# Kernel optimization log

Measured on AMD Instinct MI355X. Metric: run time of the kernel, lower is better.

The kernel has to match this reference:

```python
import jax, jax.numpy as jnp
import numpy as np

DIM, INNER, HEADS = 512, 64, 8

def setup_inputs() -> dict:
    key = jax.random.key(0)
    ks = jax.random.split(key, 9)
    s = lambda fan_in: 1.0 / np.sqrt(fan_in)
    x  = jax.random.normal(ks[0], (2, 4096, DIM), dtype=jnp.float32)
    # per-head Q/K/V projection weights (naive per-head linears in the source)
    Wq = jax.random.uniform(ks[1], (HEADS, DIM, INNER), minval=-s(DIM), maxval=s(DIM))
    Wk = jax.random.uniform(ks[2], (HEADS, DIM, INNER), minval=-s(DIM), maxval=s(DIM))
    Wv = jax.random.uniform(ks[3], (HEADS, DIM, INNER), minval=-s(DIM), maxval=s(DIM))
    bq = jax.random.uniform(ks[4], (HEADS, INNER), minval=-s(DIM), maxval=s(DIM))
    bk = jax.random.uniform(ks[5], (HEADS, INNER), minval=-s(DIM), maxval=s(DIM))
    bv = jax.random.uniform(ks[6], (HEADS, INNER), minval=-s(DIM), maxval=s(DIM))
    Wo = jax.random.uniform(ks[7], (HEADS * INNER, DIM), minval=-s(HEADS*INNER), maxval=s(HEADS*INNER))
    bo = jax.random.uniform(ks[8], (DIM,), minval=-s(HEADS*INNER), maxval=s(HEADS*INNER))
    return {"x": x, "Wq": Wq, "bq": bq, "Wk": Wk, "bk": bk, "Wv": Wv, "bv": bv, "Wo": Wo, "bo": bo}

def reference(x, Wq, bq, Wk, bk, Wv, bv, Wo, bo):
    # x: [B,S,D]; per-head projections -> [B,H,S,E]
    q = jnp.einsum('bsd,hde->bhse', x, Wq) + bq[None, :, None, :]
    k = jnp.einsum('bsd,hde->bhse', x, Wk) + bk[None, :, None, :]
    v = jnp.einsum('bsd,hde->bhse', x, Wv) + bv[None, :, None, :]
    scale = 1.0 / jnp.sqrt(jnp.asarray(q.shape[-1], q.dtype))
    scores = jnp.einsum('bhse,bhte->bhst', q, k) * scale  # [B,H,S,S]
    attn = jax.nn.softmax(scores, axis=-1)
    y = jnp.einsum('bhst,bhte->bhse', attn, v)            # [B,H,S,E]
    B, H, S, E = y.shape
    cat = jnp.transpose(y, (0, 2, 1, 3)).reshape(B, S, H * E)
    return cat @ Wo + bo
```

## Files before the change

kernel.cpp:

```cpp
#include <hip/hip_runtime.h>
#include <hip/hip_bf16.h>

typedef __attribute__((ext_vector_type(8))) short bf16x8;
typedef __attribute__((ext_vector_type(4))) float f32x4;
typedef __attribute__((ext_vector_type(16))) float f32x16;
typedef __attribute__((ext_vector_type(4))) unsigned int u32x4;

#define DIM   512
#define INNER 64
#define HEADS 8
#define BATCH 2
#define SEQ   4096
#define MTOT  (BATCH*SEQ)

__device__ __forceinline__ unsigned short f2bf(float f) {
    union { float f; unsigned u; } v; v.f = f;
    unsigned u = v.u;
    unsigned r = (u + 0x7fffu + ((u >> 16) & 1u)) >> 16;
    return (unsigned short)r;
}

__device__ __forceinline__ float bf2f(unsigned short u) {
    union { unsigned u; float f; } v; v.u = ((unsigned)u) << 16;
    return v.f;
}

__device__ __forceinline__ unsigned cvt_pk_bf16(float a, float b) {
    unsigned r;
    asm("v_cvt_pk_bf16_f32 %0, %1, %2" : "=v"(r) : "v"(a), "v"(b));
    return r;
}

#define GLOAD_LDS16(gptr, lptr)                                               \
    __builtin_amdgcn_global_load_lds(                                         \
        (const __attribute__((address_space(1))) unsigned int*)(gptr),        \
        (__attribute__((address_space(3))) unsigned int*)(lptr), 16, 0, 0)

__global__ void convert_kernel(const float* __restrict__ x,
                               const float* __restrict__ Wq,
                               const float* __restrict__ Wk,
                               const float* __restrict__ Wv,
                               const float* __restrict__ Wo,
                               unsigned short* __restrict__ xb,
                               unsigned short* __restrict__ wt,
                               unsigned short* __restrict__ wot) {
    const int total_x = MTOT * DIM / 4;
    const int total_w = 1536 * 512;
    const int total_o = 512 * 512;
    const int total   = total_x + total_w + total_o;
    for (int i = blockIdx.x * blockDim.x + threadIdx.x; i < total;
         i += gridDim.x * blockDim.x) {
        if (i < total_x) {
            float4 v = ((const float4*)x)[i];
            ushort4 o4;
            o4.x = f2bf(v.x); o4.y = f2bf(v.y); o4.z = f2bf(v.z); o4.w = f2bf(v.w);
            ((ushort4*)xb)[i] = o4;
        } else if (i < total_x + total_w) {
            int j = i - total_x;
            int n = j >> 9, d = j & 511;
            int proj = n >> 9, h = (n >> 6) & 7, e = n & 63;
            const float* W = (proj == 0) ? Wq : (proj == 1) ? Wk : Wv;
            wt[j] = f2bf(W[((size_t)h * 512 + d) * 64 + e]);
        } else {
            int j = i - total_x - total_w;
            int n = j >> 9, d = j & 511;
            wot[j] = f2bf(Wo[(size_t)d * 512 + n]);
        }
    }
}

__global__ __launch_bounds__(256) void qkv_gemm(
        const unsigned short* __restrict__ xb,
        const unsigned short* __restrict__ wt,
        const float* __restrict__ bq, const float* __restrict__ bk,
        const float* __restrict__ bv,
        unsigned short* __restrict__ Q, unsigned short* __restrict__ K,
        unsigned short* __restrict__ VT) {
    __shared__ __align__(16) unsigned short As[128][64];
    __shared__ __align__(16) unsigned short Bs[128][64];
    const int m0 = blockIdx.x * 128;
    const int n0 = blockIdx.y * 128;
    const int tid = threadIdx.x;
    const int w = tid >> 6, l = tid & 63;
    const int wm = w >> 1, wn = w & 1;
    const int srow = l >> 3;
    const int cs = (l & 7) ^ srow;
    const unsigned short* aSrc = xb + (size_t)(m0 + w * 32 + srow) * 512 + cs * 8;
    const unsigned short* bSrc = wt + (size_t)(n0 + w * 32 + srow) * 512 + cs * 8;
    f32x4 acc[4][4] = {};

    for (int k0 = 0; k0 < 512; k0 += 64) {
        __syncthreads();
        #pragma unroll
        for (int g = 0; g < 4; ++g) {
            GLOAD_LDS16(aSrc + (size_t)g * 8 * 512 + k0, &As[w * 32 + g * 8][0]);
            GLOAD_LDS16(bSrc + (size_t)g * 8 * 512 + k0, &Bs[w * 32 + g * 8][0]);
        }
        __syncthreads();
        #pragma unroll
        for (int ks = 0; ks < 2; ++ks) {
            const int ccol = (((ks * 4 + (l >> 4)) ^ (l & 7))) * 8;
            bf16x8 a[4], bb[4];
            #pragma unroll
            for (int mb = 0; mb < 4; ++mb)
                a[mb] = *(const bf16x8*)(&As[wm * 64 + mb * 16 + (l & 15)][ccol]);
            #pragma unroll
            for (int nb = 0; nb < 4; ++nb)
                bb[nb] = *(const bf16x8*)(&Bs[wn * 64 + nb * 16 + (l & 15)][ccol]);
            #pragma unroll
            for (int mb = 0; mb < 4; ++mb)
                #pragma unroll
                for (int nb = 0; nb < 4; ++nb)
                    acc[mb][nb] = __builtin_amdgcn_mfma_f32_16x16x32_bf16(
                        a[mb], bb[nb], acc[mb][nb], 0, 0, 0);
        }
    }

    const float QSCALE = 0.125f * 1.4426950408889634f;
    for (int nb = 0; nb < 4; ++nb) {
        int n = n0 + wn * 64 + nb * 16 + (l & 15);
        int proj = n >> 9, h = (n >> 6) & 7, e = n & 63;
        const float* bias = (proj == 0) ? bq : (proj == 1) ? bk : bv;
        float bval = bias[h * 64 + e];
        float scl = (proj == 0) ? QSCALE : 1.0f;
        for (int mb = 0; mb < 4; ++mb) {
            for (int r = 0; r < 4; ++r) {
                int m = m0 + wm * 64 + mb * 16 + (l >> 4) * 4 + r;
                int b = m >> 12, s = m & 4095;
                unsigned short bf = f2bf((acc[mb][nb][r] + bval) * scl);
                if (proj == 0)
                    Q[((size_t)(b * 8 + h) * 4096 + s) * 64 + e] = bf;
                else if (proj == 1)
                    K[((size_t)(b * 8 + h) * 4096 + s) * 64 + e] = bf;
                else
                    VT[((size_t)(b * 8 + h) * 64 + e) * 4096 + s] = bf;
            }
        }
    }
}

template <int NSPLIT>
__global__ __launch_bounds__(256, 4) void flash_attn(
        const unsigned short* __restrict__ Q,
        const unsigned short* __restrict__ K,
        const unsigned short* __restrict__ VT,
        unsigned short* __restrict__ y,
        unsigned short* __restrict__ Opart,
        float* __restrict__ Lpart) {
    __shared__ __align__(16) unsigned short Ks[64][64];
    __shared__ __align__(16) unsigned short Vs[64][64];

    constexpr int GRP = 16 * NSPLIT;
    const int lin = blockIdx.x;
    const int g = lin & (GRP - 1);
    const int qb = lin / GRP;
    const int bh = g / NSPLIT;
    const int z = g & (NSPLIT - 1);
    const int q0 = qb * 128;
    const int TPS = 64 / NSPLIT;
    const int t0 = z * TPS;
    const int tid = threadIdx.x;
    const int w = tid >> 6, l = tid & 63;
    const int ql = l & 31, hi = l >> 5;

    const unsigned short* Qp = Q + (size_t)bh * (4096 * 64);
    const unsigned short* Kp = K + (size_t)bh * (4096 * 64);
    const unsigned short* Vp = VT + (size_t)bh * (64 * 4096);

    bf16x8 qf[4];
    const int qrow = q0 + w * 32 + ql;
    #pragma unroll
    for (int i = 0; i < 4; ++i)
        qf[i] = *(const bf16x8*)(Qp + (size_t)qrow * 64 + i * 16 + hi * 8);

    bf16x8 ones;
    #pragma unroll
    for (int i = 0; i < 8; ++i) ones[i] = (short)0x3F80;

    const int srow = l >> 3;
    const int cs = (l & 7) ^ srow;
    const unsigned short* kSrc0 =
        Kp + ((size_t)t0 * 64 + w * 16 + srow) * 64 + cs * 8;
    const unsigned short* kSrc1 = kSrc0 + 8 * 64;
    const unsigned short* vSrc0 =
        Vp + (size_t)(w * 16 + srow) * 4096 + t0 * 64 + cs * 8;
    const unsigned short* vSrc1 = vSrc0 + 8 * 4096;

    f32x16 o[2] = {};
    f32x16 oL = {};

    for (int tt = 0; tt < TPS; ++tt) {
        {
            const size_t ko = (size_t)tt * 4096;
            const size_t vo = (size_t)tt * 64;
            GLOAD_LDS16(kSrc0 + ko, &Ks[w * 16 + 0][0]);
            GLOAD_LDS16(kSrc1 + ko, &Ks[w * 16 + 8][0]);
            GLOAD_LDS16(vSrc0 + vo, &Vs[w * 16 + 0][0]);
            GLOAD_LDS16(vSrc1 + vo, &Vs[w * 16 + 8][0]);
        }
        __syncthreads();

        #pragma unroll
        for (int kb = 0; kb < 2; ++kb) {
            f32x16 sA = {};
            __builtin_amdgcn_s_setprio(1);
            #pragma unroll
            for (int i = 0; i < 4; ++i) {
                const int chunk = (2 * i + hi) ^ (l & 7);
                bf16x8 kf = *(const bf16x8*)(&Ks[kb * 32 + ql][chunk * 8]);
                sA = __builtin_amdgcn_mfma_f32_32x32x16_bf16(kf, qf[i], sA,
                                                             0, 0, 0);
            }
            __builtin_amdgcn_s_setprio(0);

            #pragma unroll
            for (int r = 0; r < 16; ++r)
                sA[r] = __builtin_amdgcn_exp2f(sA[r]);

            bf16x8 pf0, pf1;
            {
                unsigned a0 = cvt_pk_bf16(sA[0], sA[1]);
                unsigned a1 = cvt_pk_bf16(sA[2], sA[3]);
                unsigned b0 = cvt_pk_bf16(sA[4], sA[5]);
                unsigned b1 = cvt_pk_bf16(sA[6], sA[7]);
                unsigned c0 = cvt_pk_bf16(sA[8], sA[9]);
                unsigned c1 = cvt_pk_bf16(sA[10], sA[11]);
                unsigned d0 = cvt_pk_bf16(sA[12], sA[13]);
                unsigned d1 = cvt_pk_bf16(sA[14], sA[15]);
#if __has_builtin(__builtin_amdgcn_permlane32_swap)
                auto r0 = __builtin_amdgcn_permlane32_swap(a0, b0, false, false);
                auto r1 = __builtin_amdgcn_permlane32_swap(a1, b1, false, false);
                auto r2 = __builtin_amdgcn_permlane32_swap(c0, d0, false, false);
                auto r3 = __builtin_amdgcn_permlane32_swap(c1, d1, false, false);
                u32x4 w0; w0[0] = r0[0]; w0[1] = r1[0]; w0[2] = r0[1]; w0[3] = r1[1];
                u32x4 w1; w1[0] = r2[0]; w1[1] = r3[0]; w1[2] = r2[1]; w1[3] = r3[1];
#else
                unsigned pa0 = (unsigned)__shfl_xor((int)a0, 32);
                unsigned pb0 = (unsigned)__shfl_xor((int)b0, 32);
                unsigned pa1 = (unsigned)__shfl_xor((int)a1, 32);
                unsigned pb1 = (unsigned)__shfl_xor((int)b1, 32);
                unsigned pc0 = (unsigned)__shfl_xor((int)c0, 32);
                unsigned pd0 = (unsigned)__shfl_xor((int)d0, 32);
                unsigned pc1 = (unsigned)__shfl_xor((int)c1, 32);
                unsigned pd1 = (unsigned)__shfl_xor((int)d1, 32);
                u32x4 w0, w1;
                w0[0] = hi ? pb0 : a0;  w0[1] = hi ? pb1 : a1;
                w0[2] = hi ? b0 : pa0;  w0[3] = hi ? b1 : pa1;
                w1[0] = hi ? pd0 : c0;  w1[1] = hi ? pd1 : c1;
                w1[2] = hi ? d0 : pc0;  w1[3] = hi ? d1 : pc1;
#endif
                pf0 = __builtin_bit_cast(bf16x8, w0);
                pf1 = __builtin_bit_cast(bf16x8, w1);
            }

            __builtin_amdgcn_s_setprio(1);
            #pragma unroll
            for (int eb = 0; eb < 2; ++eb) {
                const int c0i = (2 * (kb * 2 + 0) + hi) ^ (l & 7);
                const int c1i = (2 * (kb * 2 + 1) + hi) ^ (l & 7);
                bf16x8 vf0 = *(const bf16x8*)(&Vs[eb * 32 + ql][c0i * 8]);
                o[eb] = __builtin_amdgcn_mfma_f32_32x32x16_bf16(vf0, pf0, o[eb],
                                                                0, 0, 0);
                bf16x8 vf1 = *(const bf16x8*)(&Vs[eb * 32 + ql][c1i * 8]);
                o[eb] = __builtin_amdgcn_mfma_f32_32x32x16_bf16(vf1, pf1, o[eb],
                                                                0, 0, 0);
            }
            oL = __builtin_amdgcn_mfma_f32_32x32x16_bf16(ones, pf0, oL, 0, 0, 0);
            oL = __builtin_amdgcn_mfma_f32_32x32x16_bf16(ones, pf1, oL, 0, 0, 0);
            __builtin_amdgcn_s_setprio(0);
        }

        __syncthreads();
    }

    const float lsum = oL[0];

    if constexpr (NSPLIT == 1) {
        const float inv = 1.0f / lsum;
        const int bb = bh >> 3, h = bh & 7;
        unsigned short* yp = y + ((size_t)(bb * 4096 + qrow)) * 512 + h * 64;
        #pragma unroll
        for (int eb = 0; eb < 2; ++eb) {
            #pragma unroll
            for (int quad = 0; quad < 4; ++quad) {
                ushort4 pk4;
                pk4.x = f2bf(o[eb][quad * 4 + 0] * inv);
                pk4.y = f2bf(o[eb][quad * 4 + 1] * inv);
                pk4.z = f2bf(o[eb][quad * 4 + 2] * inv);
                pk4.w = f2bf(o[eb][quad * 4 + 3] * inv);
                *(ushort4*)(yp + eb * 32 + quad * 8 + hi * 4) = pk4;
            }
        }
    } else {
        const size_t prow = (size_t)z * 65536 + (size_t)bh * 4096 + qrow;
        unsigned short* op = Opart + prow * 64;
        #pragma unroll
        for (int eb = 0; eb < 2; ++eb) {
            #pragma unroll
            for (int quad = 0; quad < 4; ++quad) {
                ushort4 pk4;
                pk4.x = f2bf(o[eb][quad * 4 + 0]);
                pk4.y = f2bf(o[eb][quad * 4 + 1]);
                pk4.z = f2bf(o[eb][quad * 4 + 2]);
                pk4.w = f2bf(o[eb][quad * 4 + 3]);
                *(ushort4*)(op + eb * 32 + quad * 8 + hi * 4) = pk4;
            }
        }
        if (hi == 0) Lpart[prow] = lsum;
    }
}

template <int N>
__global__ __launch_bounds__(256) void merge_kernel(
        const unsigned short* __restrict__ Opart,
        const float* __restrict__ Lpart,
        unsigned short* __restrict__ y) {
    const int gid = blockIdx.x * 256 + threadIdx.x;
    const int row = gid >> 3;
    const int ev = gid & 7;
    float L = 0.f;
    #pragma unroll
    for (int zz = 0; zz < N; ++zz) L += Lpart[(size_t)zz * 65536 + row];
    float acc[8] = {};
    #pragma unroll
    for (int zz = 0; zz < N; ++zz) {
        const ushort4* op =
            (const ushort4*)(Opart + ((size_t)zz * 65536 + row) * 64 + ev * 8);
        ushort4 oa = op[0], ob = op[1];
        acc[0] += bf2f(oa.x); acc[1] += bf2f(oa.y);
        acc[2] += bf2f(oa.z); acc[3] += bf2f(oa.w);
        acc[4] += bf2f(ob.x); acc[5] += bf2f(ob.y);
        acc[6] += bf2f(ob.z); acc[7] += bf2f(ob.w);
    }
    const float inv = 1.0f / L;
    ushort4 ra, rb;
    ra.x = f2bf(acc[0] * inv); ra.y = f2bf(acc[1] * inv);
    ra.z = f2bf(acc[2] * inv); ra.w = f2bf(acc[3] * inv);
    rb.x = f2bf(acc[4] * inv); rb.y = f2bf(acc[5] * inv);
    rb.z = f2bf(acc[6] * inv); rb.w = f2bf(acc[7] * inv);
    const int bh = row >> 12, s = row & 4095;
    const int bb = bh >> 3, h = bh & 7;
    unsigned short* yp =
        y + ((size_t)(bb * 4096 + s)) * 512 + h * 64 + ev * 8;
    ((ushort4*)yp)[0] = ra;
    ((ushort4*)yp)[1] = rb;
}

__global__ __launch_bounds__(256) void out_gemm(
        const unsigned short* __restrict__ yb,
        const unsigned short* __restrict__ wot,
        const float* __restrict__ bo,
        float* __restrict__ out) {
    __shared__ __align__(16) unsigned short As[128][64];
    __shared__ __align__(16) unsigned short Bs[128][64];
    const int m0 = blockIdx.x * 128;
    const int n0 = blockIdx.y * 128;
    const int tid = threadIdx.x;
    const int w = tid >> 6, l = tid & 63;
    const int wm = w >> 1, wn = w & 1;
    const int srow = l >> 3;
    const int cs = (l & 7) ^ srow;
    const unsigned short* aSrc = yb + (size_t)(m0 + w * 32 + srow) * 512 + cs * 8;
    const unsigned short* bSrc = wot + (size_t)(n0 + w * 32 + srow) * 512 + cs * 8;
    f32x4 acc[4][4] = {};

    for (int k0 = 0; k0 < 512; k0 += 64) {
        __syncthreads();
        #pragma unroll
        for (int g = 0; g < 4; ++g) {
            GLOAD_LDS16(aSrc + (size_t)g * 8 * 512 + k0, &As[w * 32 + g * 8][0]);
            GLOAD_LDS16(bSrc + (size_t)g * 8 * 512 + k0, &Bs[w * 32 + g * 8][0]);
        }
        __syncthreads();
        #pragma unroll
        for (int ks = 0; ks < 2; ++ks) {
            const int ccol = (((ks * 4 + (l >> 4)) ^ (l & 7))) * 8;
            bf16x8 a[4], bb[4];
            #pragma unroll
            for (int mb = 0; mb < 4; ++mb)
                a[mb] = *(const bf16x8*)(&As[wm * 64 + mb * 16 + (l & 15)][ccol]);
            #pragma unroll
            for (int nb = 0; nb < 4; ++nb)
                bb[nb] = *(const bf16x8*)(&Bs[wn * 64 + nb * 16 + (l & 15)][ccol]);
            #pragma unroll
            for (int mb = 0; mb < 4; ++mb)
                #pragma unroll
                for (int nb = 0; nb < 4; ++nb)
                    acc[mb][nb] = __builtin_amdgcn_mfma_f32_16x16x32_bf16(
                        a[mb], bb[nb], acc[mb][nb], 0, 0, 0);
        }
    }

    for (int nb = 0; nb < 4; ++nb) {
        int n = n0 + wn * 64 + nb * 16 + (l & 15);
        float bval = bo[n];
        for (int mb = 0; mb < 4; ++mb) {
            for (int r = 0; r < 4; ++r) {
                int m = m0 + wm * 64 + mb * 16 + (l >> 4) * 4 + r;
                out[(size_t)m * 512 + n] = acc[mb][nb][r] + bval;
            }
        }
    }
}

extern "C" void kernel_launch(void* const* d_in, const int* in_sizes, int n_in,
                              void* d_out, int out_size, void* d_ws,
                              size_t ws_size, hipStream_t stream) {
    const float* x  = (const float*)d_in[0];
    const float* Wq = (const float*)d_in[1];
    const float* bq = (const float*)d_in[2];
    const float* Wk = (const float*)d_in[3];
    const float* bk = (const float*)d_in[4];
    const float* Wv = (const float*)d_in[5];
    const float* bv = (const float*)d_in[6];
    const float* Wo = (const float*)d_in[7];
    const float* bo = (const float*)d_in[8];
    float* out = (float*)d_out;

    char* ws = (char*)d_ws;
    unsigned short* xb  = (unsigned short*)(ws);
    unsigned short* wt  = (unsigned short*)(ws + 8388608);
    unsigned short* wot = (unsigned short*)(ws + 9961472);
    unsigned short* Qb  = (unsigned short*)(ws + 10485760);
    unsigned short* Kb  = (unsigned short*)(ws + 18874368);
    unsigned short* VTb = (unsigned short*)(ws + 27262976);
    unsigned short* yb  = (unsigned short*)(ws + 35651584);
    float* Lpart = (float*)(ws + 44040192);
    unsigned short* Opart = (unsigned short*)(ws + 45088768);
    const size_t need2 = 45088768 + 2ull * 8388608;

    hipLaunchKernelGGL(convert_kernel, dim3(1024), dim3(256), 0, stream,
                       x, Wq, Wk, Wv, Wo, xb, wt, wot);
    hipLaunchKernelGGL(qkv_gemm, dim3(64, 12), dim3(256), 0, stream,
                       xb, wt, bq, bk, bv, Qb, Kb, VTb);
    if (ws_size >= need2) {
        hipLaunchKernelGGL((flash_attn<2>), dim3(32 * 16 * 2), dim3(256), 0,
                           stream, Qb, Kb, VTb, yb, Opart, Lpart);
        hipLaunchKernelGGL((merge_kernel<2>), dim3(2048), dim3(256), 0, stream,
                           Opart, Lpart, yb);
    } else {
        hipLaunchKernelGGL((flash_attn<1>), dim3(32 * 16), dim3(256), 0,
                           stream, Qb, Kb, VTb, yb, (unsigned short*)nullptr,
                           (float*)nullptr);
    }
    hipLaunchKernelGGL(out_gemm, dim3(64, 4), dim3(256), 0, stream,
                       yb, wot, bo, out);
}
```

Baseline: 139.4 us.

## Double attention KV tile to 128 keys and tile-transpose weight conversion

The flash attention kernel now stages 128 keys per iteration instead of 64, which halves the number of load/barrier rounds per split and processes four 32-key sub-blocks between syncs. The V tile gets a new XOR swizzle to match the wider layout. Separately, the weight conversion now transposes through a shared-memory tile so global reads and writes are coalesced instead of strided. The cost is twice the LDS footprint in attention, which may lower occupancy under the 4-blocks launch bound. The diff is partial: the V reads inside the loop must also change to the new layout.

Result: faster. 135.6 us (-2.8%).

```diff
diff --git a/kernel.cpp b/kernel.cpp
--- a/kernel.cpp
+++ b/kernel.cpp
@@ -36,35 +36,54 @@
         (const __attribute__((address_space(1))) unsigned int*)(gptr),        \
         (__attribute__((address_space(3))) unsigned int*)(lptr), 16, 0, 0)
 
-__global__ void convert_kernel(const float* __restrict__ x,
-                               const float* __restrict__ Wq,
-                               const float* __restrict__ Wk,
-                               const float* __restrict__ Wv,
-                               const float* __restrict__ Wo,
-                               unsigned short* __restrict__ xb,
-                               unsigned short* __restrict__ wt,
-                               unsigned short* __restrict__ wot) {
-    const int total_x = MTOT * DIM / 4;
-    const int total_w = 1536 * 512;
-    const int total_o = 512 * 512;
-    const int total   = total_x + total_w + total_o;
-    for (int i = blockIdx.x * blockDim.x + threadIdx.x; i < total;
-         i += gridDim.x * blockDim.x) {
-        if (i < total_x) {
+__global__ __launch_bounds__(256) void convert_kernel(
+        const float* __restrict__ x,
+        const float* __restrict__ Wq,
+        const float* __restrict__ Wk,
+        const float* __restrict__ Wv,
+        const float* __restrict__ Wo,
+        unsigned short* __restrict__ xb,
+        unsigned short* __restrict__ wt,
+        unsigned short* __restrict__ wot) {
+    const int blk = blockIdx.x;
+    const int tid = threadIdx.x;
+    if (blk < 256) {
+        __shared__ float tile[64][65];
+        const int r4 = tid >> 2;
+        const int c16 = (tid & 3) * 16;
+        if (blk < 192) {
+            const int proj = blk / 64, rem = blk % 64;
+            const int h = rem / 8, d0 = (rem % 8) * 64;
+            const float* W = (proj == 0) ? Wq : (proj == 1) ? Wk : Wv;
+            const float* src = W + ((size_t)h * 512 + d0) * 64;
+            #pragma unroll
+            for (int j = 0; j < 16; ++j)
+                tile[r4][c16 + j] = src[(size_t)r4 * 64 + c16 + j];
+            __syncthreads();
+            unsigned short* o =
+                wt + ((size_t)(proj * 512 + h * 64 + r4)) * 512 + d0 + c16;
+            #pragma unroll
+            for (int j = 0; j < 16; ++j)
+                o[j] = f2bf(tile[c16 + j][r4]);
+        } else {
+            const int t2 = blk - 192;
+            const int d0 = (t2 >> 3) * 64, n0 = (t2 & 7) * 64;
+            #pragma unroll
+            for (int j = 0; j < 16; ++j)
+                tile[r4][c16 + j] = Wo[(size_t)(d0 + r4) * 512 + n0 + c16 + j];
+            __syncthreads();
+            unsigned short* o = wot + ((size_t)(n0 + r4)) * 512 + d0 + c16;
+            #pragma unroll
+            for (int j = 0; j < 16; ++j)
+                o[j] = f2bf(tile[c16 + j][r4]);
+        }
+    } else {
+        const int total_x = MTOT * DIM / 4;
+        for (int i = (blk - 256) * 256 + tid; i < total_x; i += 768 * 256) {
             float4 v = ((const float4*)x)[i];
             ushort4 o4;
             o4.x = f2bf(v.x); o4.y = f2bf(v.y); o4.z = f2bf(v.z); o4.w = f2bf(v.w);
             ((ushort4*)xb)[i] = o4;
-        } else if (i < total_x + total_w) {
-            int j = i - total_x;
-            int n = j >> 9, d = j & 511;
-            int proj = n >> 9, h = (n >> 6) & 7, e = n & 63;
-            const float* W = (proj == 0) ? Wq : (proj == 1) ? Wk : Wv;
-            wt[j] = f2bf(W[((size_t)h * 512 + d) * 64 + e]);
-        } else {
-            int j = i - total_x - total_w;
-            int n = j >> 9, d = j & 511;
-            wot[j] = f2bf(Wo[(size_t)d * 512 + n]);
         }
     }
 }
@@ -147,8 +166,8 @@
         unsigned short* __restrict__ y,
         unsigned short* __restrict__ Opart,
         float* __restrict__ Lpart) {
-    __shared__ __align__(16) unsigned short Ks[64][64];
-    __shared__ __align__(16) unsigned short Vs[64][64];
+    __shared__ __align__(16) unsigned short Ks[128][64];
+    __shared__ __align__(16) unsigned short Vs[64][128];
 
     constexpr int GRP = 16 * NSPLIT;
     const int lin = blockIdx.x;
@@ -157,7 +176,7 @@
     const int bh = g / NSPLIT;
     const int z = g & (NSPLIT - 1);
     const int q0 = qb * 128;
-    const int TPS = 64 / NSPLIT;
+    const int TPS = 32 / NSPLIT;
     const int t0 = z * TPS;
     const int tid = threadIdx.x;
     const int w = tid >> 6, l = tid & 63;
@@ -178,30 +197,45 @@
     for (int i = 0; i < 8; ++i) ones[i] = (short)0x3F80;
 
     const int srow = l >> 3;
-    const int cs = (l & 7) ^ srow;
-    const unsigned short* kSrc0 =
-        Kp + ((size_t)t0 * 64 + w * 16 + srow) * 64 + cs * 8;
-    const unsigned short* kSrc1 = kSrc0 + 8 * 64;
-    const unsigned short* vSrc0 =
-        Vp + (size_t)(w * 16 + srow) * 4096 + t0 * 64 + cs * 8;
-    const unsigned short* vSrc1 = vSrc0 + 8 * 4096;
+    const int csk = (l & 7) ^ srow;
+    const unsigned short* kSrcB =
+        Kp + ((size_t)t0 * 128 + w * 32 + srow) * 64 + csk * 8;
+
+    const int vsub = l >> 4;
+    const int vc = l & 15;
+    const unsigned short* vS0;
+    const unsigned short* vS1;
+    const unsigned short* vS2;
+    const unsigned short* vS3;
+    {
+        const int r0 = w * 16 + 0 + vsub, r1 = w * 16 + 4 + vsub;
+        const int r2 = w * 16 + 8 + vsub, r3 = w * 16 + 12 + vsub;
+        vS0 = Vp + (size_t)r0 * 4096 + (size_t)t0 * 128 + (vc ^ (r0 & 7)) * 8;
+        vS1 = Vp + (size_t)r1 * 4096 + (size_t)t0 * 128 + (vc ^ (r1 & 7)) * 8;
+        vS2 = Vp + (size_t)r2 * 4096 + (size_t)t0 * 128 + (vc ^ (r2 & 7)) * 8;
+        vS3 = Vp + (size_t)r3 * 4096 + (size_t)t0 * 128 + (vc ^ (r3 & 7)) * 8;
+    }
 
     f32x16 o[2] = {};
     f32x16 oL = {};
 
     for (int tt = 0; tt < TPS; ++tt) {
         {
-            const size_t ko = (size_t)tt * 4096;
-            const size_t vo = (size_t)tt * 64;
-            GLOAD_LDS16(kSrc0 + ko, &Ks[w * 16 + 0][0]);
-            GLOAD_LDS16(kSrc1 + ko, &Ks[w * 16 + 8][0]);
-            GLOAD_LDS16(vSrc0 + vo, &Vs[w * 16 + 0][0]);
-            GLOAD_LDS16(vSrc1 + vo, &Vs[w * 16 + 8][0]);
-        }
-        __syncthreads();
-
-        #pragma unroll
-        for (int kb = 0; kb < 2; ++kb) {
+            const size_t ko = (size_t)tt * 128 * 64;
+            const size_t vo = (size_t)tt * 128;
+            GLOAD_LDS16(kSrcB + ko + 0 * 8 * 64, &Ks[w * 32 + 0][0]);
+            GLOAD_LDS16(kSrcB + ko + 1 * 8 * 64, &Ks[w * 32 + 8][0]);
+            GLOAD_LDS16(kSrcB + ko + 2 * 8 * 64, &Ks[w * 32 + 16][0]);
+            GLOAD_LDS16(kSrcB + ko + 3 * 8 * 64, &Ks[w * 32 + 24][0]);
+            GLOAD_LDS16(vS0 + vo, &Vs[w * 16 + 0][0]);
+            GLOAD_LDS16(vS1 + vo, &Vs[w * 16 + 4][0]);
+            GLOAD_LDS16(vS2 + vo, &Vs[w * 16 + 8][0]);
+            GLOAD_LDS16(vS3 + vo, &Vs[w * 16 + 12][0]);
+        }
+        __syncthreads();
+
+        #pragma unroll
+        for (int kb = 0; kb < 4; ++kb) {
             f32x16 sA = {};
             __builtin_amdgcn_s_setprio(1);
             #pragma unroll
```
